# Kernel tuning notes

Hardware: AMD Instinct MI355X
Metric: run time of the kernel (lower is better)

Reference implementation:

```python
import jax, jax.numpy as jnp
import numpy as np

N, CIN, OUT, G, K = 16, 128, 128, 8, 56
GP = OUT // G  # group_planes = 16
EPS = 1e-5


def _bn(x, gamma, beta, mean, var, caxis):
    # inference-mode batchnorm over channel axis `caxis`
    shape = [1] * x.ndim
    shape[caxis] = x.shape[caxis]
    g = gamma.reshape(shape)
    b = beta.reshape(shape)
    m = mean.reshape(shape)
    v = var.reshape(shape)
    return (x - m) * (g * jax.lax.rsqrt(v + EPS)) + b


def setup_inputs() -> dict:
    key = jax.random.key(0)
    ks = jax.random.split(key, 16)
    d = {}
    d['x'] = jax.random.normal(ks[0], (N, CIN, K, K), jnp.float32)
    d['w_qkv'] = jax.random.normal(ks[1], (2 * OUT, CIN), jnp.float32) * np.float32(np.sqrt(1.0 / CIN))
    d['relative'] = jax.random.normal(ks[2], (2 * GP, 2 * K - 1), jnp.float32) * np.float32(np.sqrt(1.0 / GP))

    def bn_params(k, c):
        k1, k2, k3, k4 = jax.random.split(k, 4)
        gamma = 1.0 + 0.1 * jax.random.normal(k1, (c,), jnp.float32)
        beta = 0.05 * jax.random.normal(k2, (c,), jnp.float32)
        mean = 0.05 * jax.random.normal(k3, (c,), jnp.float32)
        var = 1.0 + 0.1 * jax.random.uniform(k4, (c,), jnp.float32)
        return gamma, beta, mean, var

    d['qkv_gamma'], d['qkv_beta'], d['qkv_mean'], d['qkv_var'] = bn_params(ks[3], 2 * OUT)
    d['sim_gamma'], d['sim_beta'], d['sim_mean'], d['sim_var'] = bn_params(ks[4], 3 * G)
    d['out_gamma'], d['out_beta'], d['out_mean'], d['out_var'] = bn_params(ks[5], 2 * OUT)
    return d


def reference(x, w_qkv, relative,
              qkv_gamma, qkv_beta, qkv_mean, qkv_var,
              sim_gamma, sim_beta, sim_mean, sim_var,
              out_gamma, out_beta, out_mean, out_var):
    n, c, h, w = x.shape  # width=False: attend along H
    xb = jnp.transpose(x, (0, 3, 1, 2)).reshape(n * w, c, h)  # [B, C, H], B = N*W

    # 1x1 conv qkv + BN1d
    qkv = jnp.einsum('oc,bch->boh', w_qkv, xb)  # [B, 2*OUT, H]
    qkv = _bn(qkv, qkv_gamma, qkv_beta, qkv_mean, qkv_var, 1)
    qkv = qkv.reshape(n * w, G, 2 * GP, h)
    hp = GP // 2
    q, k, v = qkv[:, :, :hp], qkv[:, :, hp:2 * hp], qkv[:, :, 2 * hp:]

    # relative position embeddings
    qi = jnp.arange(K)[None, :]
    ki = jnp.arange(K)[:, None]
    flat_idx = (ki - qi + K - 1).reshape(-1)  # [K*K]
    all_emb = relative[:, flat_idx].reshape(2 * GP, K, K)
    q_emb, k_emb, v_emb = all_emb[:hp], all_emb[hp:2 * hp], all_emb[2 * hp:]

    qr = jnp.einsum('bgci,cij->bgij', q, q_emb)
    kr = jnp.einsum('bgci,cij->bgij', k, k_emb).transpose(0, 1, 3, 2)
    qk = jnp.einsum('bgci,bgcj->bgij', q, k)

    stacked = jnp.concatenate([qk, qr, kr], axis=1)  # [B, 3G, H, H]
    stacked = _bn(stacked, sim_gamma, sim_beta, sim_mean, sim_var, 1)
    sim = stacked.reshape(n * w, 3, G, h, h).sum(axis=1)  # [B, G, H, H]
    sim = jax.nn.softmax(sim, axis=3)

    sv = jnp.einsum('bgij,bgcj->bgci', sim, v)      # [B, G, GP, H]
    sve = jnp.einsum('bgij,cij->bgci', sim, v_emb)  # [B, G, GP, H]
    # torch cat(dim=-1) then view(B, 2*OUT, H) == stack on a new axis before H
    stacked_out = jnp.concatenate([sv[:, :, :, None, :], sve[:, :, :, None, :]], axis=3)
    stacked_out = stacked_out.reshape(n * w, 2 * OUT, h)
    out = _bn(stacked_out, out_gamma, out_beta, out_mean, out_var, 1)
    out = out.reshape(n, w, OUT, 2, h).sum(axis=3)  # [N, W, OUT, H]
    out = jnp.transpose(out, (0, 2, 3, 1))  # [N, OUT, H, W]
    return out
```

## Files before the change

kernel.cpp:

```cpp
#include <hip/hip_runtime.h>
#include <hip/hip_bf16.h>
#include <cstddef>

#define EPSV 1e-5f

typedef __attribute__((ext_vector_type(8))) short bf16x8;
typedef __attribute__((ext_vector_type(4))) float f32x4;
typedef __attribute__((ext_vector_type(4))) short short4v;
typedef __attribute__((ext_vector_type(4))) int int4v;

__device__ __forceinline__ float b2f(short s) {
  union { unsigned u; float f; } x;
  x.u = ((unsigned)(unsigned short)s) << 16;
  return x.f;
}
__device__ __forceinline__ short f2b(float f) {
  union { __hip_bfloat16 h; short s; } x;
  x.h = __float2bfloat16(f);
  return x.s;
}

#define PF_W    3300000
#define PF_RQ   3316384
#define PF_RK   3327136
#define PF_RV   3337888
#define PF_QSC  3346592
#define PF_QSH  3346848
#define PF_OSC  3347104
#define PF_OSH  3347360
#define PF_SH3  3347616

__global__ __launch_bounds__(256) void k_prep(
    const float* __restrict__ wq, const float* __restrict__ rel,
    const float* __restrict__ qg, const float* __restrict__ qb,
    const float* __restrict__ qm, const float* __restrict__ qv,
    const float* __restrict__ sg, const float* __restrict__ sb,
    const float* __restrict__ sm, const float* __restrict__ svar,
    const float* __restrict__ og, const float* __restrict__ ob,
    const float* __restrict__ om, const float* __restrict__ ov,
    float* __restrict__ prep) {
  const int g = blockIdx.x;
  const int tid = threadIdx.x;
  const float scA = sg[g] * rsqrtf(svar[g] + EPSV);
  const float scB = sg[8 + g] * rsqrtf(svar[8 + g] + EPSV);
  const float scC = sg[16 + g] * rsqrtf(svar[16 + g] + EPSV);
  const float rCA = scC / scA;

  short* wb = (short*)(prep + PF_W) + g * 4096;
  for (int t = tid; t < 1024; t += 256) {
    int o = t >> 5, c0 = (t & 31) * 4;
    float4 wv = *(const float4*)&wq[g * 4096 + o * 128 + c0];
    short4v s4 = {f2b(wv.x), f2b(wv.y), f2b(wv.z), f2b(wv.w)};
    *(short4v*)&wb[o * 128 + c0] = s4;
  }
  float* rq = prep + PF_RQ + g * 1344;
  float* rk = prep + PF_RK + g * 1344;
  for (int t = tid; t < 1344; t += 256) {
    int d = t / 12, c = t - d * 12;
    rq[t] = (c < 8 && d < 111) ? rel[c * 111 + d] * scB : 0.f;
    rk[t] = (c < 8 && d < 111) ? rel[(8 + c) * 111 + d] * rCA : 0.f;
  }
  short* rv = (short*)(prep + PF_RV) + g * 2176;
  for (int t = tid; t < 2176; t += 256) {
    int c = t / 136, d = t - c * 136;
    rv[t] = (d < 111) ? f2b(rel[(16 + c) * 111 + d]) : (short)0;
  }
  if (tid < 32) {
    int ch = g * 32 + tid;
    float sc = qg[ch] * rsqrtf(qv[ch] + EPSV);
    float sh = qb[ch] - qm[ch] * sc;
    if (tid >= 8 && tid < 16) { sc *= scA; sh *= scA; }
    prep[PF_QSC + ch] = sc;
    prep[PF_QSH + ch] = sh;
    float so = og[ch] * rsqrtf(ov[ch] + EPSV);
    prep[PF_OSC + ch] = so;
    prep[PF_OSH + ch] = ob[ch] - om[ch] * so;
  }
  if (tid == 0) {
    float shA = sb[g] - sm[g] * scA;
    float shB = sb[8 + g] - sm[8 + g] * scB;
    float shC = sb[16 + g] - sm[16 + g] * scC;
    prep[PF_SH3 + g] = shA + shB + shC;
  }
}

__global__ __launch_bounds__(256) void k_transpose_in(const float* __restrict__ x,
                                                      unsigned* __restrict__ xbT) {
  const int nh = blockIdx.x;
  const int n = nh / 56, h = nh - n * 56;
  __shared__ short t2[128 * 57];
  const float* src = x + (size_t)n * 401408 + h * 56;
  for (int t = threadIdx.x; t < 1792; t += 256) {
    int c = t / 14, w4 = (t - c * 14) * 4;
    float4 v = *(const float4*)&src[c * 3136 + w4];
    t2[c * 57 + w4 + 0] = f2b(v.x);
    t2[c * 57 + w4 + 1] = f2b(v.y);
    t2[c * 57 + w4 + 2] = f2b(v.z);
    t2[c * 57 + w4 + 3] = f2b(v.w);
  }
  __syncthreads();
  for (int t = threadIdx.x; t < 3584; t += 256) {
    int w = t >> 6, cp = t & 63;
    unsigned lo = (unsigned short)t2[(2 * cp) * 57 + w];
    unsigned hi = (unsigned short)t2[(2 * cp + 1) * 57 + w];
    xbT[(((size_t)(n * 56 + w) * 56 + h) << 6) + cp] = lo | (hi << 16);
  }
}

__global__ __launch_bounds__(256) void k_transpose_out(const float* __restrict__ tmp,
                                                       float* __restrict__ out) {
  int nc = blockIdx.x;
  int n = nc >> 7, c = nc & 127;
  __shared__ float t[56][57];
  for (int idx = threadIdx.x; idx < 3136; idx += 256) {
    int w = idx / 56, h = idx - w * 56;
    t[h][w] = tmp[((size_t)(n * 56 + w) * 128 + c) * 56 + h];
  }
  __syncthreads();
  float* dst = out + (size_t)nc * 3136;
  for (int idx = threadIdx.x; idx < 3136; idx += 256)
    dst[idx] = t[idx / 56][idx % 56];
}

#define O_XST    0
#define O_SHFT   0
#define O_WS     7680
#define O_SIMA   7680
#define O_QKT    12288
#define O_SVL    12288
#define O_RQTF   14528
#define O_RKTF   17216
#define O_RELV   19904
#define O_VBH    22080
#define O_VBL    23232
#define SB_SH    24384

__global__ __launch_bounds__(512) void k_fused(
    const short* __restrict__ xbT, const float* __restrict__ prep,
    float* __restrict__ tmp) {
  const int tid = threadIdx.x;
  const int g = blockIdx.x / 896;
  const int b = blockIdx.x - g * 896;

  __shared__ __align__(16) short SB[SB_SH];
  __shared__ float s_qsc[32], s_qsh[32], s_osc[32], s_osh[32], s_sh3;

  const int lane = tid & 63;
  const int w = tid >> 6;
  const int m = lane & 15;
  const int qd = lane >> 4;
  const int it = w >> 1;
  const int half = w & 1;
  const int grp = tid >> 4;
  const int l16 = tid & 15;

  {
    int4v z = {0, 0, 0, 0};
    int4v* zp = (int4v*)(SB + O_VBH);
    for (int i = tid; i < 288; i += 512) zp[i] = z;

    const short* xsrc = xbT + (size_t)b * 7168;
    for (int t = tid; t < 896; t += 512) {
      int h = t >> 4, ck = (t & 15) * 8;
      *(bf16x8*)&SB[O_XST + h * 136 + ck] = *(const bf16x8*)&xsrc[h * 128 + ck];
    }
    const short* wsrc = (const short*)(prep + PF_W) + g * 4096;
    for (int t = tid; t < 512; t += 512) {
      int o = t >> 4, ck = (t & 15) * 8;
      *(bf16x8*)&SB[O_WS + o * 136 + ck] = *(const bf16x8*)&wsrc[o * 128 + ck];
    }
    const f32x4* rqp = (const f32x4*)(prep + PF_RQ + g * 1344);
    const f32x4* rkp = (const f32x4*)(prep + PF_RK + g * 1344);
    f32x4* rqd = (f32x4*)(SB + O_RQTF);
    f32x4* rkd = (f32x4*)(SB + O_RKTF);
    for (int t = tid; t < 672; t += 512) {
      if (t < 336) rqd[t] = rqp[t];
      else         rkd[t - 336] = rkp[t - 336];
    }
    const int4v* rvp = (const int4v*)((const short*)(prep + PF_RV) + g * 2176);
    int4v* rvd = (int4v*)(SB + O_RELV);
    for (int t = tid; t < 272; t += 512) rvd[t] = rvp[t];
    if (tid < 32) {
      s_qsc[tid] = prep[PF_QSC + g * 32 + tid];
      s_qsh[tid] = prep[PF_QSH + g * 32 + tid];
      s_osc[tid] = prep[PF_OSC + g * 32 + tid];
      s_osh[tid] = prep[PF_OSH + g * 32 + tid];
    }
    if (tid == 0) s_sh3 = prep[PF_SH3 + g];
  }
  __syncthreads();

  {
    const int o = half * 16 + m;
    const int h = it * 16 + m;
    f32x4 acc = {0.f, 0.f, 0.f, 0.f};
#pragma unroll
    for (int ks = 0; ks < 4; ++ks) {
      bf16x8 av = *(bf16x8*)&SB[O_WS + o * 136 + qd * 8 + ks * 32];
      bf16x8 bv = *(bf16x8*)&SB[O_XST + h * 136 + qd * 8 + ks * 32];
      acc = __builtin_amdgcn_mfma_f32_16x16x32_bf16(av, bv, acc, 0, 0, 0);
    }
    if (h < 56) {
      float* qkTf = (float*)(SB + O_QKT);
      if (half == 0) {
        float4 o4;
        o4.x = fmaf(acc[0], s_qsc[qd * 4 + 0], s_qsh[qd * 4 + 0]);
        o4.y = fmaf(acc[1], s_qsc[qd * 4 + 1], s_qsh[qd * 4 + 1]);
        o4.z = fmaf(acc[2], s_qsc[qd * 4 + 2], s_qsh[qd * 4 + 2]);
        o4.w = fmaf(acc[3], s_qsc[qd * 4 + 3], s_qsh[qd * 4 + 3]);
        *(float4*)&qkTf[h * 20 + qd * 4] = o4;
      } else {
#pragma unroll
        for (int r = 0; r < 4; ++r) {
          int cv = qd * 4 + r;
          float val = fmaf(acc[r], s_qsc[16 + cv], s_qsh[16 + cv]);
          short vh = f2b(val);
          short vl = f2b(val - b2f(vh));
          SB[O_VBH + cv * 72 + h] = vh;
          SB[O_VBL + cv * 72 + h] = vl;
        }
      }
    }
  }
  __syncthreads();

  {
    const float* qkTf = (const float*)(SB + O_QKT);
    const float* rqf = (const float*)(SB + O_RQTF);
    const float* rkf = (const float*)(SB + O_RKTF);
    const float sh3 = s_sh3;
    const int4v z = {0, 0, 0, 0};

    float4 kv0[4], kv1[4];
#pragma unroll
    for (int jt = 0; jt < 4; ++jt) {
      int j = jt * 16 + l16;
      int jj = (j < 56) ? j : 0;
      kv0[jt] = *(const float4*)&qkTf[jj * 20 + 8];
      kv1[jt] = *(const float4*)&qkTf[jj * 20 + 12];
    }

#pragma unroll
    for (int pass = 0; pass < 2; ++pass) {
      int i = pass * 32 + grp;
      if (i < 64 && l16 < 15) *(int4v*)&SB[O_SHFT + i * 120 + l16 * 8] = z;
      if (i < 56) {
        float4 qa = *(const float4*)&qkTf[i * 20 + 0];
        float4 qb4 = *(const float4*)&qkTf[i * 20 + 4];
        float L[4];
#pragma unroll
        for (int jt = 0; jt < 4; ++jt) {
          int j = jt * 16 + l16;
          if (j < 56) {
            const float4 rq0 = *(const float4*)&rqf[(i - j + 55) * 12];
            const float4 rq1 = *(const float4*)&rqf[(i - j + 55) * 12 + 4];
            const float4 rk0 = *(const float4*)&rkf[(j - i + 55) * 12];
            const float4 rk1 = *(const float4*)&rkf[(j - i + 55) * 12 + 4];
            const float4 k0 = kv0[jt], k1 = kv1[jt];
            float acc = sh3;
            acc = fmaf(qa.x, k0.x, acc);  acc = fmaf(qa.y, k0.y, acc);
            acc = fmaf(qa.z, k0.z, acc);  acc = fmaf(qa.w, k0.w, acc);
            acc = fmaf(qb4.x, k1.x, acc); acc = fmaf(qb4.y, k1.y, acc);
            acc = fmaf(qb4.z, k1.z, acc); acc = fmaf(qb4.w, k1.w, acc);
            acc = fmaf(qa.x, rq0.x, acc);  acc = fmaf(qa.y, rq0.y, acc);
            acc = fmaf(qa.z, rq0.z, acc);  acc = fmaf(qa.w, rq0.w, acc);
            acc = fmaf(qb4.x, rq1.x, acc); acc = fmaf(qb4.y, rq1.y, acc);
            acc = fmaf(qb4.z, rq1.z, acc); acc = fmaf(qb4.w, rq1.w, acc);
            acc = fmaf(k0.x, rk0.x, acc);  acc = fmaf(k0.y, rk0.y, acc);
            acc = fmaf(k0.z, rk0.z, acc);  acc = fmaf(k0.w, rk0.w, acc);
            acc = fmaf(k1.x, rk1.x, acc);  acc = fmaf(k1.y, rk1.y, acc);
            acc = fmaf(k1.w, rk1.w, acc);  acc = fmaf(k1.z, rk1.z, acc);
            L[jt] = acc;
          } else {
            L[jt] = -3.0e38f;
          }
        }
        float mx = fmaxf(fmaxf(L[0], L[1]), fmaxf(L[2], L[3]));
#pragma unroll
        for (int off = 1; off < 16; off <<= 1) mx = fmaxf(mx, __shfl_xor(mx, off));
        float sum = 0.f, ex[4];
#pragma unroll
        for (int jt = 0; jt < 4; ++jt) {
          ex[jt] = __expf(L[jt] - mx);
          sum += ex[jt];
        }
#pragma unroll
        for (int off = 1; off < 16; off <<= 1) sum += __shfl_xor(sum, off);
        float inv = 1.0f / sum;
#pragma unroll
        for (int jt = 0; jt < 4; ++jt) {
          int j = jt * 16 + l16;
          if (j < 56) {
            short pv = f2b(ex[jt] * inv);
            SB[O_SIMA + i * 72 + j] = pv;
            SB[O_SHFT + i * 120 + (i - j + 55)] = pv;
          } else {
            SB[O_SIMA + i * 72 + j] = 0;
          }
        }
      }
    }
  }
  __syncthreads();

  f32x4 sveacc = {0.f, 0.f, 0.f, 0.f};
  {
    if (half == 0) {
      bf16x8 pa0 = *(bf16x8*)&SB[O_SIMA + (it * 16 + m) * 72 + qd * 8];
      bf16x8 pa1 = *(bf16x8*)&SB[O_SIMA + (it * 16 + m) * 72 + qd * 8 + 32];
      f32x4 acc = {0.f, 0.f, 0.f, 0.f};
      bf16x8 bv;
      bv = *(bf16x8*)&SB[O_VBH + m * 72 + qd * 8];
      acc = __builtin_amdgcn_mfma_f32_16x16x32_bf16(pa0, bv, acc, 0, 0, 0);
      bv = *(bf16x8*)&SB[O_VBH + m * 72 + qd * 8 + 32];
      acc = __builtin_amdgcn_mfma_f32_16x16x32_bf16(pa1, bv, acc, 0, 0, 0);
      bv = *(bf16x8*)&SB[O_VBL + m * 72 + qd * 8];
      acc = __builtin_amdgcn_mfma_f32_16x16x32_bf16(pa0, bv, acc, 0, 0, 0);
      bv = *(bf16x8*)&SB[O_VBL + m * 72 + qd * 8 + 32];
      acc = __builtin_amdgcn_mfma_f32_16x16x32_bf16(pa1, bv, acc, 0, 0, 0);
      float* svLf = (float*)(SB + O_SVL);
#pragma unroll
      for (int r = 0; r < 4; ++r) {
        int i2 = it * 16 + qd * 4 + r;
        if (i2 < 56) svLf[m * 60 + i2] = acc[r];
      }
    } else {
#pragma unroll
      for (int ks = 0; ks < 4; ++ks) {
        bf16x8 av = *(bf16x8*)&SB[O_RELV + m * 136 + qd * 8 + ks * 32];
        bf16x8 bv = *(bf16x8*)&SB[O_SHFT + (it * 16 + m) * 120 + qd * 8 + ks * 32];
        sveacc = __builtin_amdgcn_mfma_f32_16x16x32_bf16(av, bv, sveacc, 0, 0, 0);
      }
    }
  }
  __syncthreads();

  if (half == 1) {
    const int i2 = it * 16 + m;
    if (i2 < 56) {
      const float* svLf = (const float*)(SB + O_SVL);
#pragma unroll
      for (int r = 0; r < 4; ++r) {
        int c = qd * 4 + r;
        float svv = svLf[c * 60 + i2];
        float o = fmaf(svv, s_osc[2 * c], s_osh[2 * c]) +
                  fmaf(sveacc[r], s_osc[2 * c + 1], s_osh[2 * c + 1]);
        tmp[((size_t)b * 128 + g * 16 + c) * 56 + i2] = o;
      }
    }
  }
}

extern "C" void kernel_launch(void* const* d_in, const int* in_sizes, int n_in,
                              void* d_out, int out_size, void* d_ws, size_t ws_size,
                              hipStream_t stream) {
  const float* x   = (const float*)d_in[0];
  const float* wq  = (const float*)d_in[1];
  const float* rel = (const float*)d_in[2];
  const float* qg = (const float*)d_in[3];
  const float* qb = (const float*)d_in[4];
  const float* qm = (const float*)d_in[5];
  const float* qv = (const float*)d_in[6];
  const float* sg = (const float*)d_in[7];
  const float* sb = (const float*)d_in[8];
  const float* sm = (const float*)d_in[9];
  const float* sv = (const float*)d_in[10];
  const float* og = (const float*)d_in[11];
  const float* ob = (const float*)d_in[12];
  const float* om = (const float*)d_in[13];
  const float* ov = (const float*)d_in[14];
  float* out = (float*)d_out;

  float* tmp = (float*)d_ws;

  k_prep<<<8, 256, 0, stream>>>(wq, rel, qg, qb, qm, qv,
                                sg, sb, sm, sv, og, ob, om, ov, out);
  k_transpose_in<<<896, 256, 0, stream>>>(x, (unsigned*)out);
  k_fused<<<7168, 512, 0, stream>>>((const short*)out, out, tmp);
  k_transpose_out<<<2048, 256, 0, stream>>>(tmp, out);
}
```

Measured before the change: 115.0 us.

## Compute relative-position qr/kr logits with MFMA over all offsets then gather

Replaces the per-(i,j) scalar FMA evaluation of the q·r_q and k·r_k relative terms with MFMA products of q/k (split into bf16 hi/lo pairs) against every relative offset. The products go into shared-memory tables that are then gathered along the diagonals. This moves work from the FMA pipes onto the matrix units. In exchange it adds shared-memory staging, two extra MFMA phases, several extra barriers and a reload of the relative tables, and it uses a bf16 split whose precision may differ slightly.

Result: slower. 127.7 us (+11.0%).

```diff
diff --git a/kernel.cpp b/kernel.cpp
--- a/kernel.cpp
+++ b/kernel.cpp
@@ -21,14 +21,14 @@
 }
 
 #define PF_W    3300000
-#define PF_RQ   3316384
-#define PF_RK   3327136
-#define PF_RV   3337888
-#define PF_QSC  3346592
-#define PF_QSH  3346848
-#define PF_OSC  3347104
-#define PF_OSH  3347360
-#define PF_SH3  3347616
+#define PF_RQP  3316384
+#define PF_RKP  3334304
+#define PF_RV   3352224
+#define PF_QSC  3360928
+#define PF_QSH  3361184
+#define PF_OSC  3361440
+#define PF_OSH  3361696
+#define PF_SH3  3361952
 
 __global__ __launch_bounds__(256) void k_prep(
     const float* __restrict__ wq, const float* __restrict__ rel,
@@ -53,12 +53,17 @@
     short4v s4 = {f2b(wv.x), f2b(wv.y), f2b(wv.z), f2b(wv.w)};
     *(short4v*)&wb[o * 128 + c0] = s4;
   }
-  float* rq = prep + PF_RQ + g * 1344;
-  float* rk = prep + PF_RK + g * 1344;
-  for (int t = tid; t < 1344; t += 256) {
-    int d = t / 12, c = t - d * 12;
-    rq[t] = (c < 8 && d < 111) ? rel[c * 111 + d] * scB : 0.f;
-    rk[t] = (c < 8 && d < 111) ? rel[(8 + c) * 111 + d] * rCA : 0.f;
+  short* rqp = (short*)(prep + PF_RQP) + g * 4480;
+  short* rkp = (short*)(prep + PF_RKP) + g * 4480;
+  for (int t = tid; t < 4480; t += 256) {
+    int d = t / 40, c = t - d * 40;
+    short vq = 0, vk = 0;
+    if (d < 111) {
+      if (c < 16) vq = f2b(rel[(c & 7) * 111 + d] * scB);
+      else if (c < 32) vk = f2b(rel[(8 + (c & 7)) * 111 + d] * rCA);
+    }
+    rqp[t] = vq;
+    rkp[t] = vk;
   }
   short* rv = (short*)(prep + PF_RV) + g * 2176;
   for (int t = tid; t < 2176; t += 256) {
@@ -123,17 +128,17 @@
 }
 
 #define O_XST    0
+#define O_WS     7616
 #define O_SHFT   0
-#define O_WS     7680
 #define O_SIMA   7680
-#define O_QKT    12288
-#define O_SVL    12288
-#define O_RQTF   14528
-#define O_RKTF   17216
-#define O_RELV   19904
-#define O_VBH    22080
-#define O_VBL    23232
-#define SB_SH    24384
+#define O_QKT    12656
+#define O_SVL    12656
+#define O_QKA    14896
+#define O_RB     17456
+#define O_RELV   17456
+#define O_VBH    21936
+#define O_VBL    23088
+#define SB_SH    24240
 
 __global__ __launch_bounds__(512) void k_fused(
     const short* __restrict__ xbT, const float* __restrict__ prep,
@@ -169,17 +174,9 @@
       int o = t >> 4, ck = (t & 15) * 8;
       *(bf16x8*)&SB[O_WS + o * 136 + ck] = *(const bf16x8*)&wsrc[o * 128 + ck];
     }
-    const f32x4* rqp = (const f32x4*)(prep + PF_RQ + g * 1344);
-    const f32x4* rkp = (const f32x4*)(prep + PF_RK + g * 1344);
-    f32x4* rqd = (f32x4*)(SB + O_RQTF);
-    f32x4* rkd = (f32x4*)(SB + O_RKTF);
-    for (int t = tid; t < 672; t += 512) {
-      if (t < 336) rqd[t] = rqp[t];
-      else         rkd[t - 336] = rkp[t - 336];
-    }
-    const int4v* rvp = (const int4v*)((const short*)(prep + PF_RV) + g * 2176);
-    int4v* rvd = (int4v*)(SB + O_RELV);
-    for (int t = tid; t < 272; t += 512) rvd[t] = rvp[t];
+    const int4v* rqsrc = (const int4v*)((const short*)(prep + PF_RQP) + g * 4480);
+    int4v* rbd = (int4v*)(SB + O_RB);
+    for (int t = tid; t < 560; t += 512) rbd[t] = rqsrc[t];
     if (tid < 32) {
       s_qsc[tid] = prep[PF_QSC + g * 32 + tid];
       s_qsh[tid] = prep[PF_QSH + g * 32 + tid];
@@ -203,12 +200,25 @@
     if (h < 56) {
       float* qkTf = (float*)(SB + O_QKT);
       if (half == 0) {
-        float4 o4;
-        o4.x = fmaf(acc[0], s_qsc[qd * 4 + 0], s_qsh[qd * 4 + 0]);
-        o4.y = fmaf(acc[1], s_qsc[qd * 4 + 1], s_qsh[qd * 4 + 1]);
-        o4.z = fmaf(acc[2], s_qsc[qd * 4 + 2], s_qsh[qd * 4 + 2]);
-        o4.w = fmaf(acc[3], s_qsc[qd * 4 + 3], s_qsh[qd * 4 + 3]);
+        float v4[4];
+#pragma unroll
+        for (int r = 0; r < 4; ++r)
+          v4[r] = fmaf(acc[r], s_qsc[qd * 4 + r], s_qsh[qd * 4 + r]);
+        float4 o4 = {v4[0], v4[1], v4[2], v4[3]};
         *(float4*)&qkTf[h * 20 + qd * 4] = o4;
+#pragma unroll
+        for (int r = 0; r < 4; ++r) {
+          int oo = qd * 4 + r;
+          short vh = f2b(v4[r]);
+          short vl = f2b(v4[r] - b2f(vh));
+          if (oo < 8) {
+            SB[O_QKA + h * 40 + oo] = vh;
+            SB[O_QKA + h * 40 + 8 + oo] = vl;
+          } else {
+            SB[O_QKA + h * 40 + 8 + oo] = vh;
+            SB[O_QKA + h * 40 + 16 + oo] = vl;
+          }
+        }
       } else {
 #pragma unroll
         for (int r = 0; r < 4; ++r) {
@@ -224,13 +234,60 @@
   }
   __syncthreads();
 
+  float* Tf = (float*)SB;
+  for (int tau = w; tau < 28; tau += 8) {
+    int itT = tau / 7, ct = tau - itT * 7;
+    bf16x8 av = *(bf16x8*)&SB[O_QKA + (itT * 16 + m) * 40 + qd * 8];
+    bf16x8 bv = *(bf16x8*)&SB[O_RB + (ct * 16 + m) * 40 + qd * 8];
+    f32x4 t0 = {0.f, 0.f, 0.f, 0.f};
+    t0 = __builtin_amdgcn_mfma_f32_16x16x32_bf16(av, bv, t0, 0, 0, 0);
+#pragma unroll
+    for (int r = 0; r < 4; ++r) {
+      int i2 = itT * 16 + qd * 4 + r;
+      if (i2 < 56) Tf[i2 * 113 + ct * 16 + m] = t0[r];
+    }
+  }
+  __syncthreads();
+
+  float qr_reg[2][4];
+#pragma unroll
+  for (int pass = 0; pass < 2; ++pass) {
+    int i = pass * 32 + grp;
+#pragma unroll
+    for (int jt = 0; jt < 4; ++jt) {
+      int j = jt * 16 + l16;
+      qr_reg[pass][jt] = (i < 56 && j < 56) ? Tf[i * 113 + (i - j + 55)] : 0.f;
+    }
+  }
+  {
+    const int4v* rksrc = (const int4v*)((const short*)(prep + PF_RKP) + g * 4480);
+    int4v* rbd = (int4v*)(SB + O_RB);
+    for (int t = tid; t < 560; t += 512) rbd[t] = rksrc[t];
+  }
+  __syncthreads();
+
+  float* UTf = (float*)SB;
+  for (int tau = w; tau < 28; tau += 8) {
+    int itT = tau / 7, ct = tau - itT * 7;
+    bf16x8 av = *(bf16x8*)&SB[O_QKA + (itT * 16 + m) * 40 + qd * 8];
+    bf16x8 bv = *(bf16x8*)&SB[O_RB + (ct * 16 + m) * 40 + qd * 8];
+    f32x4 t0 = {0.f, 0.f, 0.f, 0.f};
+    t0 = __builtin_amdgcn_mfma_f32_16x16x32_bf16(av, bv, t0, 0, 0, 0);
+    int d = ct * 16 + m;
+    if (d < 111) {
+#pragma unroll
+      for (int r = 0; r < 4; ++r) {
+        int j2 = itT * 16 + qd * 4 + r;
+        if (j2 < 56) UTf[d * 57 + j2] = t0[r];
+      }
+    }
+  }
+  __syncthreads();
+
+  float P[2][4];
   {
     const float* qkTf = (const float*)(SB + O_QKT);
-    const float* rqf = (const float*)(SB + O_RQTF);
-    const float* rkf = (const float*)(SB + O_RKTF);
     const float sh3 = s_sh3;
-    const int4v z = {0, 0, 0, 0};
-
     float4 kv0[4], kv1[4];
 #pragma unroll
     for (int jt = 0; jt < 4; ++jt) {
@@ -239,11 +296,9 @@
       kv0[jt] = *(const float4*)&qkTf[jj * 20 + 8];
       kv1[jt] = *(const float4*)&qkTf[jj * 20 + 12];
     }
-
 #pragma unroll
     for (int pass = 0; pass < 2; ++pass) {
       int i = pass * 32 + grp;
-      if (i < 64 && l16 < 15) *(int4v*)&SB[O_SHFT + i * 120 + l16 * 8] = z;
       if (i < 56) {
         float4 qa = *(const float4*)&qkTf[i * 20 + 0];
         float4 qb4 = *(const float4*)&qkTf[i * 20 + 4];
@@ -252,24 +307,13 @@
         for (int jt = 0; jt < 4; ++jt) {
           int j = jt * 16 + l16;
           if (j < 56) {
-            const float4 rq0 = *(const float4*)&rqf[(i - j + 55) * 12];
-            const float4 rq1 = *(const float4*)&rqf[(i - j + 55) * 12 + 4];
-            const float4 rk0 = *(const float4*)&rkf[(j - i + 55) * 12];
-            const float4 rk1 = *(const float4*)&rkf[(j - i + 55) * 12 + 4];
+            float krv = UTf[(j - i + 55) * 57 + j];
             const float4 k0 = kv0[jt], k1 = kv1[jt];
-            float acc = sh3;
+            float acc = sh3 + qr_reg[pass][jt] + krv;
             acc = fmaf(qa.x, k0.x, acc);  acc = fmaf(qa.y, k0.y, acc);
             acc = fmaf(qa.z, k0.z, acc);  acc = fmaf(qa.w, k0.w, acc);
             acc = fmaf(qb4.x, k1.x, acc); acc = fmaf(qb4.y, k1.y, acc);
             acc = fmaf(qb4.z, k1.z, acc); acc = fmaf(qb4.w, k1.w, acc);
-            acc = fmaf(qa.x, rq0.x, acc);  acc = fmaf(qa.y, rq0.y, acc);
-            acc = fmaf(qa.z, rq0.z, acc);  acc = fmaf(qa.w, rq0.w, acc);
-            acc = fmaf(qb4.x, rq1.x, acc); acc = fmaf(qb4.y, rq1.y, acc);
-            acc = fmaf(qb4.z, rq1.z, acc); acc = fmaf(qb4.w, rq1.w, acc);
-            acc = fmaf(k0.x, rk0.x, acc);  acc = fmaf(k0.y, rk0.y, acc);
-            acc = fmaf(k0.z, rk0.z, acc);  acc = fmaf(k0.w, rk0.w, acc);
-            acc = fmaf(k1.x, rk1.x, acc);  acc = fmaf(k1.y, rk1.y, acc);
-            acc = fmaf(k1.w, rk1.w, acc);  acc = fmaf(k1.z, rk1.z, acc);
             L[jt] = acc;
           } else {
             L[jt] = -3.0e38f;
@@ -288,10 +332,24 @@
         for (int off = 1; off < 16; off <<= 1) sum += __shfl_xor(sum, off);
         float inv = 1.0f / sum;
 #pragma unroll
+        for (int jt = 0; jt < 4; ++jt) P[pass][jt] = ex[jt] * inv;
+      }
+    }
+  }
+  __syncthreads();
+
+  {
+    const int4v z = {0, 0, 0, 0};
+#pragma unroll
+    for (int pass = 0; pass < 2; ++pass) {
+      int i = pass * 32 + grp;
+      if (l16 < 15) *(int4v*)&SB[O_SHFT + i * 120 + l16 * 8] = z;
+      if (i < 56) {
+#pragma unroll
         for (int jt = 0; jt < 4; ++jt) {
           int j = jt * 16 + l16;
           if (j < 56) {
-            short pv = f2b(ex[jt] * inv);
+            short pv = f2b(P[pass][jt]);
             SB[O_SIMA + i * 72 + j] = pv;
             SB[O_SHFT + i * 120 + (i - j + 55)] = pv;
           } else {
@@ -300,6 +358,9 @@
         }
       }
     }
+    const int4v* rvp = (const int4v*)((const short*)(prep + PF_RV) + g * 2176);
+    int4v* rvd = (int4v*)(SB + O_RELV);
+    for (int t = tid; t < 272; t += 512) rvd[t] = rvp[t];
   }
   __syncthreads();
 
```
